# Kernel tuning notes

Hardware: AMD Instinct MI355X
Metric: run time of the kernel (lower is better)

The kernel has to match this reference:

```python
import jax, jax.numpy as jnp
import numpy as np

B = 32768
SEQ_LEN = 24
H = 64            # HIDDEN_DIM
SLOTS = 8         # MEMORY_SLOTS
VOCAB = 64        # VOCAB_SIZE


def setup_inputs() -> dict:
    key = jax.random.key(0)
    ks = jax.random.split(key, 8)
    seqs = jax.random.randint(ks[0], (B, SEQ_LEN), 0, VOCAB, dtype=jnp.int64)
    query_tok = jax.random.randint(ks[1], (B,), 0, VOCAB + 2, dtype=jnp.int64)
    embed = jax.random.normal(ks[2], (VOCAB + 2, H), dtype=jnp.float32) * 0.05
    gw1 = jax.random.normal(ks[3], (2 * H, 32), dtype=jnp.float32) / np.sqrt(2 * H)
    gb1 = jnp.zeros((32,), jnp.float32)
    gw2 = jax.random.normal(ks[4], (32, 1), dtype=jnp.float32) / np.sqrt(32)
    gb2 = jnp.zeros((1,), jnp.float32)
    rw1 = jax.random.normal(ks[5], (2 * H, H), dtype=jnp.float32) / np.sqrt(2 * H)
    rb1 = jnp.zeros((H,), jnp.float32)
    rw2 = jax.random.normal(ks[6], (H, VOCAB), dtype=jnp.float32) / np.sqrt(H)
    rb2 = jnp.zeros((VOCAB,), jnp.float32)
    return {"seqs": seqs, "query_tok": query_tok, "embed": embed,
            "gw1": gw1, "gb1": gb1, "gw2": gw2, "gb2": gb2,
            "rw1": rw1, "rb1": rb1, "rw2": rw2, "rb2": rb2}


def reference(seqs, query_tok, embed, gw1, gb1, gw2, gb2, rw1, rb1, rw2, rb2):
    Bb = seqs.shape[0]
    T = SEQ_LEN - 1  # model writes tokens 0..SEQ_LEN-2 into memory
    embs = embed[seqs[:, :T]]                     # [B, T, H]
    batch_idx = jnp.arange(Bb)

    def step(mem, xs):
        t, emb = xs                               # emb: [B, H]
        ctx = jnp.broadcast_to(emb[:, None, :], mem.shape)
        pair = jnp.concatenate([ctx, mem], axis=-1)        # [B, S, 2H]
        h = jax.nn.relu(pair @ gw1 + gb1)                  # [B, S, 32]
        score = jax.nn.sigmoid(h @ gw2 + gb2)[..., 0]      # [B, S]
        # while memory not full, fill slot t; otherwise evict argmax score
        idx = jnp.where(t < SLOTS, t, jnp.argmax(score, axis=1))
        mem = mem.at[batch_idx, idx].set(emb)
        return mem, None

    mem0 = jnp.zeros((Bb, SLOTS, H), embed.dtype)
    mem, _ = jax.lax.scan(step, mem0, (jnp.arange(T), jnp.swapaxes(embs, 0, 1)))

    summary = mem.mean(axis=1)                    # [B, H]  (memory is full: T > SLOTS)
    q = embed[query_tok]                          # [B, H]
    x = jnp.concatenate([q, summary], axis=-1)    # [B, 2H]
    logits = jax.nn.relu(x @ rw1 + rb1) @ rw2 + rb2   # [B, VOCAB]
    return logits
```

## Files before the change

### kernel.cpp

```cpp
#include <hip/hip_runtime.h>
#include <math.h>

typedef __attribute__((ext_vector_type(8))) _Float16 f16x8;
typedef __attribute__((ext_vector_type(4))) float f32x4;

#define TSTEPS 23
#define ROWS 128

#define WSB_Z  0
#define WSB_B1 16384
#define WSB_W2 37888

__global__ __launch_bounds__(256) void pre_all(
    const float* __restrict__ embed, const float* __restrict__ gw1,
    const float* __restrict__ gb1, const float* __restrict__ gw2,
    const float* __restrict__ gb2, const float* __restrict__ rw1,
    const float* __restrict__ rb1, const float* __restrict__ rw2,
    char* __restrict__ wsc)
{
    __shared__ float sEmb[66 * 64];
    __shared__ float sW[128 * 64];
    __shared__ float sV[64 * 33];
    __shared__ float sU[4 * 32];
    __shared__ float sG[65];
    __shared__ float sRb1[64];

    const int tid = threadIdx.x;
    const int blk = blockIdx.x;

    if (blk < 16) {
        {
            const float4* es = (const float4*)embed;
            float4* ed = (float4*)sEmb;
            for (int i = tid; i < 1024; i += 256) ed[i] = es[i];
            const float4* gs = (const float4*)gw1;
            float4* gd = (float4*)sW;
            for (int i = tid; i < 1024; i += 256) gd[i] = gs[i];
            if (tid < 32) { sG[tid] = gb1[tid]; sG[32 + tid] = gw2[tid]; }
            if (tid == 64) sG[64] = gb2[0];
        }
        __syncthreads();
        {
            const int s = tid >> 2, j0 = (tid & 3) * 8;
            float4 er[16];
            const float4* erp = (const float4*)(sEmb + s * 64);
            #pragma unroll
            for (int q = 0; q < 16; ++q) er[q] = erp[q];
            float acc[8] = {0.f, 0.f, 0.f, 0.f, 0.f, 0.f, 0.f, 0.f};
            #pragma unroll
            for (int k = 0; k < 64; ++k) {
                const float ek = ((const float*)er)[k];
                const float4 w0 = *(const float4*)&sW[(64 + k) * 32 + j0];
                const float4 w1 = *(const float4*)&sW[(64 + k) * 32 + j0 + 4];
                acc[0] = fmaf(ek, w0.x, acc[0]); acc[1] = fmaf(ek, w0.y, acc[1]);
                acc[2] = fmaf(ek, w0.z, acc[2]); acc[3] = fmaf(ek, w0.w, acc[3]);
                acc[4] = fmaf(ek, w1.x, acc[4]); acc[5] = fmaf(ek, w1.y, acc[5]);
                acc[6] = fmaf(ek, w1.z, acc[6]); acc[7] = fmaf(ek, w1.w, acc[7]);
            }
            #pragma unroll
            for (int jj = 0; jj < 8; ++jj) sV[s * 33 + j0 + jj] = acc[jj];
        }
        if (tid < 128) {
            const int cc = tid >> 5, j = tid & 31;
            const int c = blk * 4 + cc;
            float acc = 0.f;
            const float* er = sEmb + c * 64;
            #pragma unroll
            for (int k = 0; k < 64; ++k)
                acc = fmaf(er[k], sW[k * 32 + j], acc);
            sU[cc * 32 + j] = acc;
        }
        __syncthreads();
        {
            const int cc = tid >> 6, s = tid & 63;
            const int c = blk * 4 + cc;
            double z = (double)sG[64];
            #pragma unroll
            for (int j = 0; j < 32; ++j) {
                const double a = (double)sU[cc * 32 + j] + (double)sV[s * 33 + j] + (double)sG[j];
                if (a > 0.0) z += a * (double)sG[32 + j];
            }
            ((float*)(wsc + WSB_Z))[c * 64 + s] = (float)(1.0 / (1.0 + exp(-z)));
        }
    } else if (blk < 49) {
        {
            const float4* es = (const float4*)embed;
            float4* ed = (float4*)sEmb;
            for (int i = tid; i < 1056; i += 256) ed[i] = es[i];
            const float4* rs = (const float4*)rw1;
            float4* rd = (float4*)sW;
            for (int i = tid; i < 2048; i += 256) rd[i] = rs[i];
            if (tid < 64) sRb1[tid] = rb1[tid];
        }
        __syncthreads();
        const int e = (blk - 16) * 256 + tid;
        if (e < 8320) {
            const int n = e & 63, k = e >> 6;
            const int trow = (k < 64) ? k : (k - 64);
            const int ofs = (k < 64) ? 64 : 0;
            float4 er[16];
            const float4* erp = (const float4*)(sEmb + trow * 64);
            #pragma unroll
            for (int q = 0; q < 16; ++q) er[q] = erp[q];
            float acc = (k < 64) ? 0.f : sRb1[n];
            #pragma unroll
            for (int m = 0; m < 64; ++m)
                acc = fmaf(((const float*)er)[m], sW[(ofs + m) * 64 + n], acc);
            acc *= (k < 64) ? (0.125f * 256.f) : 256.f;
            ((_Float16*)(wsc + WSB_B1))[n * 168 + k] = (_Float16)acc;
        }
    } else {
        _Float16* w2t = (_Float16*)(wsc + WSB_W2);
        for (int e = tid; e < 4096; e += 256) {
            const int n = e & 63, j = e >> 6;
            w2t[n * 72 + j] = (_Float16)rw2[j * 64 + n];
        }
        _Float16* b1 = (_Float16*)(wsc + WSB_B1);
        for (int e = tid; e < 2432; e += 256) {
            const int n = e / 38, k = 130 + (e - n * 38);
            b1[n * 168 + k] = (_Float16)0.f;
        }
    }
}

__device__ __forceinline__ f16x8 build_slot_win(const unsigned* s, const unsigned* hb, int ko)
{
    unsigned w0 = 0, w1 = 0, w2 = 0, w3 = 0;
    #pragma unroll
    for (int i = 0; i < 8; ++i) {
        const unsigned d = s[i] - (unsigned)ko;
        const unsigned val = (d < 8u) ? (hb[i] << ((d & 1u) * 16)) : 0u;
        const unsigned q = d >> 1;
        w0 |= (q == 0u) ? val : 0u;
        w1 |= (q == 1u) ? val : 0u;
        w2 |= (q == 2u) ? val : 0u;
        w3 |= (q == 3u) ? val : 0u;
    }
    union { unsigned u[4]; f16x8 v; } r;
    r.u[0] = w0; r.u[1] = w1; r.u[2] = w2; r.u[3] = w3;
    return r.v;
}

__device__ __forceinline__ f16x8 build_q_win(int kq, int ko)
{
    const unsigned d = (unsigned)(kq - ko);
    const unsigned val = (d < 8u) ? (0x3C00u << ((d & 1u) * 16)) : 0u;
    const unsigned q = d >> 1;
    union { unsigned u[4]; f16x8 v; } r;
    r.u[0] = (q == 0u) ? val : 0u;
    r.u[1] = (q == 1u) ? val : 0u;
    r.u[2] = (q == 2u) ? val : 0u;
    r.u[3] = (q == 3u) ? val : 0u;
    return r.v;
}

#define L_Z    0
#define L_B1   16384
#define L_W2   37888
#define L_H    47104
#define L_ROW  65536
#define L_RB2  67584

__global__ __launch_bounds__(512, 4) void sm_main(
    const int* __restrict__ seqs, const int* __restrict__ qtok,
    const float* __restrict__ rb2, const char* __restrict__ wsc,
    float* __restrict__ out)
{
    __shared__ __align__(16) char smem[67840];
    float*    sZ   = (float*)(smem + L_Z);
    _Float16* sB1  = (_Float16*)(smem + L_B1);
    _Float16* sW2  = (_Float16*)(smem + L_W2);
    _Float16* sH   = (_Float16*)(smem + L_H);
    uint4*    sRow = (uint4*)(smem + L_ROW);
    float*    sRb2 = (float*)(smem + L_RB2);

    const int tid = threadIdx.x;
    const int base = blockIdx.x * ROWS;

    unsigned pk[6];
    int qt = 0;
    if (tid < ROWS) {
        const int4* sq = (const int4*)(seqs + (size_t)(base + tid) * 24);
        #pragma unroll
        for (int i = 0; i < 6; ++i) {
            const int4 w4 = sq[i];
            pk[i] = (unsigned)w4.x | ((unsigned)w4.y << 8) |
                    ((unsigned)w4.z << 16) | ((unsigned)w4.w << 24);
        }
        qt = qtok[base + tid];
    }

    {
        const float4* zsrc = (const float4*)(wsc + WSB_Z);
        float4* zdst = (float4*)sZ;
        for (int i = tid; i < 1024; i += 512) zdst[i] = zsrc[i];
        const float4* b1s = (const float4*)(wsc + WSB_B1);
        float4* b1d = (float4*)sB1;
        for (int i = tid; i < 1344; i += 512) b1d[i] = b1s[i];
        const float4* w2s = (const float4*)(wsc + WSB_W2);
        float4* w2d = (float4*)sW2;
        for (int i = tid; i < 576; i += 512) w2d[i] = w2s[i];
        if (tid < 64) sRb2[tid] = rb2[tid];
    }
    __syncthreads();

    if (tid < ROWS) {
        unsigned lo = pk[0], hi = pk[1];
        #pragma unroll
        for (int t = 8; t < TSTEPS; ++t) {
            const int c = (int)((pk[t >> 2] >> ((t & 3) * 8)) & 255u);
            const float* zr = sZ + c * 64;
            float b = zr[lo & 63]; int am = 0; float z;
            z = zr[(lo >> 8) & 63];  if (z > b) { b = z; am = 1; }
            z = zr[(lo >> 16) & 63]; if (z > b) { b = z; am = 2; }
            z = zr[lo >> 24];        if (z > b) { b = z; am = 3; }
            z = zr[hi & 63];         if (z > b) { b = z; am = 4; }
            z = zr[(hi >> 8) & 63];  if (z > b) { b = z; am = 5; }
            z = zr[(hi >> 16) & 63]; if (z > b) { b = z; am = 6; }
            z = zr[hi >> 24];        if (z > b) { b = z; am = 7; }
            const unsigned cb = (unsigned)c;
            if (am < 4) { const int sh = am * 8; lo = (lo & ~(255u << sh)) | (cb << sh); }
            else        { const int sh = am * 8 - 32; hi = (hi & ~(255u << sh)) | (cb << sh); }
        }
        int t_[8] = { (int)(lo & 63), (int)((lo >> 8) & 63), (int)((lo >> 16) & 63), (int)(lo >> 24),
                      (int)(hi & 63), (int)((hi >> 8) & 63), (int)((hi >> 16) & 63), (int)(hi >> 24) };
        int tot[8] = {1, 1, 1, 1, 1, 1, 1, 1};
        #pragma unroll
        for (int i = 0; i < 8; ++i)
            #pragma unroll
            for (int j = i + 1; j < 8; ++j) {
                const int eq = (t_[i] == t_[j]);
                tot[i] += eq; tot[j] += eq;
            }
        unsigned tp = 0;
        #pragma unroll
        for (int i = 0; i < 8; ++i) tp |= (unsigned)tot[i] << (4 * i);
        sRow[tid] = make_uint4(lo & 0x3F3F3F3Fu, hi & 0x3F3F3F3Fu, tp, (unsigned)qt);
    }
    __syncthreads();

    const int lane = tid & 63;
    const int w = tid >> 6;
    const int c16 = lane & 15, g = lane >> 4;
    const int arow = w * 16 + c16;

    unsigned sl[8], hb[8];
    int kq;
    {
        const uint4 ri = sRow[arow];
        sl[0] = ri.x & 63u; sl[1] = (ri.x >> 8) & 63u;
        sl[2] = (ri.x >> 16) & 63u; sl[3] = ri.x >> 24;
        sl[4] = ri.y & 63u; sl[5] = (ri.y >> 8) & 63u;
        sl[6] = (ri.y >> 16) & 63u; sl[7] = ri.y >> 24;
        #pragma unroll
        for (int i = 0; i < 8; ++i) {
            const unsigned tot = (ri.z >> (4 * i)) & 15u;
            union { _Float16 h; unsigned short b; } cv;
            cv.h = (_Float16)(float)tot;
            hb[i] = (unsigned)cv.b;
        }
        kq = 64 + (int)ri.w;
    }

    f32x4 a0 = {0.f, 0.f, 0.f, 0.f}, a1 = a0, a2 = a0, a3 = a0;
    #pragma unroll
    for (int ks = 0; ks < 5; ++ks) {
        const int ko = ks * 32 + g * 8;
        const f16x8 af = (ks < 2) ? build_slot_win(sl, hb, ko) : build_q_win(kq, ko);
        const f16x8 b0 = *(const f16x8*)&sB1[(c16) * 168 + ko];
        const f16x8 b1 = *(const f16x8*)&sB1[(16 + c16) * 168 + ko];
        const f16x8 b2 = *(const f16x8*)&sB1[(32 + c16) * 168 + ko];
        const f16x8 b3 = *(const f16x8*)&sB1[(48 + c16) * 168 + ko];
        a0 = __builtin_amdgcn_mfma_f32_16x16x32_f16(af, b0, a0, 0, 0, 0);
        a1 = __builtin_amdgcn_mfma_f32_16x16x32_f16(af, b1, a1, 0, 0, 0);
        a2 = __builtin_amdgcn_mfma_f32_16x16x32_f16(af, b2, a2, 0, 0, 0);
        a3 = __builtin_amdgcn_mfma_f32_16x16x32_f16(af, b3, a3, 0, 0, 0);
    }
    {
        const int rbase = w * 16 + g * 4;
        #pragma unroll
        for (int j = 0; j < 4; ++j) {
            _Float16* hr = sH + (rbase + j) * 72;
            const float v0 = a0[j], v1 = a1[j], v2 = a2[j], v3 = a3[j];
            hr[c16]      = (_Float16)(v0 > 0.f ? v0 : 0.f);
            hr[16 + c16] = (_Float16)(v1 > 0.f ? v1 : 0.f);
            hr[32 + c16] = (_Float16)(v2 > 0.f ? v2 : 0.f);
            hr[48 + c16] = (_Float16)(v3 > 0.f ? v3 : 0.f);
        }
    }
    __syncthreads();

    f32x4 d0 = {0.f, 0.f, 0.f, 0.f}, d1 = d0, d2 = d0, d3 = d0;
    #pragma unroll
    for (int ks = 0; ks < 2; ++ks) {
        const int ko = ks * 32 + g * 8;
        const f16x8 af = *(const f16x8*)&sH[arow * 72 + ko];
        const f16x8 b0 = *(const f16x8*)&sW2[(c16) * 72 + ko];
        const f16x8 b1 = *(const f16x8*)&sW2[(16 + c16) * 72 + ko];
        const f16x8 b2 = *(const f16x8*)&sW2[(32 + c16) * 72 + ko];
        const f16x8 b3 = *(const f16x8*)&sW2[(48 + c16) * 72 + ko];
        d0 = __builtin_amdgcn_mfma_f32_16x16x32_f16(af, b0, d0, 0, 0, 0);
        d1 = __builtin_amdgcn_mfma_f32_16x16x32_f16(af, b1, d1, 0, 0, 0);
        d2 = __builtin_amdgcn_mfma_f32_16x16x32_f16(af, b2, d2, 0, 0, 0);
        d3 = __builtin_amdgcn_mfma_f32_16x16x32_f16(af, b3, d3, 0, 0, 0);
    }
    float* sOut = (float*)(void*)smem;
    {
        const int rbase = w * 16 + g * 4;
        #pragma unroll
        for (int j = 0; j < 4; ++j) {
            float* orow = sOut + (rbase + j) * 68;
            orow[c16]      = d0[j] * (1.f / 256.f) + sRb2[c16];
            orow[16 + c16] = d1[j] * (1.f / 256.f) + sRb2[16 + c16];
            orow[32 + c16] = d2[j] * (1.f / 256.f) + sRb2[32 + c16];
            orow[48 + c16] = d3[j] * (1.f / 256.f) + sRb2[48 + c16];
        }
    }
    __syncthreads();

    #pragma unroll
    for (int r2 = 0; r2 < 4; ++r2) {
        const int idx = r2 * 512 + tid;
        const int row = idx >> 4, c4 = idx & 15;
        *(float4*)(out + (size_t)(base + row) * 64 + c4 * 4) =
            *(const float4*)&sOut[row * 68 + c4 * 4];
    }
}

extern "C" void kernel_launch(void* const* d_in, const int* in_sizes, int n_in,
                              void* d_out, int out_size, void* d_ws, size_t ws_size,
                              hipStream_t stream)
{
    const int* seqs    = (const int*)d_in[0];
    const int* qtok    = (const int*)d_in[1];
    const float* embed = (const float*)d_in[2];
    const float* gw1   = (const float*)d_in[3];
    const float* gb1   = (const float*)d_in[4];
    const float* gw2   = (const float*)d_in[5];
    const float* gb2   = (const float*)d_in[6];
    const float* rw1   = (const float*)d_in[7];
    const float* rb1   = (const float*)d_in[8];
    const float* rw2   = (const float*)d_in[9];
    const float* rb2   = (const float*)d_in[10];
    char* wsc  = (char*)d_ws;
    float* out = (float*)d_out;
    const int B = in_sizes[1];

    pre_all<<<50, 256, 0, stream>>>(embed, gw1, gb1, gw2, gb2, rw1, rb1, rw2, wsc);
    sm_main<<<B / ROWS, 512, 0, stream>>>(seqs, qtok, rb2, wsc, out);
}
```

Baseline: 21.44 us.

## Split gate-score precompute into two kernels and overlap weight staging with eviction scan

The gate-score table precompute is split in two. The first kernel computes the per-token U and V projections with one thread per output. A second small kernel combines them into the score table with four independent double accumulators, and it stores the pre-sigmoid logit, which keeps the same argmax ordering. In the main kernel only the score table is loaded before the first barrier, and the idle threads 128-511 stage the MLP weights while the first 128 threads run the eviction scan. This adds one more kernel launch in exchange for a shorter dependency chain and less serialized loading.

After: 22.30 us. 1.04x slower.

```diff
diff --git a/kernel.cpp b/kernel.cpp
--- a/kernel.cpp
+++ b/kernel.cpp
@@ -7,22 +7,19 @@
 #define TSTEPS 23
 #define ROWS 128
 
-#define WSB_Z  0
-#define WSB_B1 16384
-#define WSB_W2 37888
-
-__global__ __launch_bounds__(256) void pre_all(
+#define WSB_B1 0
+#define WSB_W2 21504
+#define WSB_U  30720
+#define WSB_V  38912
+#define WSB_Z  47104
+
+__global__ __launch_bounds__(256) void pre_lite(
     const float* __restrict__ embed, const float* __restrict__ gw1,
-    const float* __restrict__ gb1, const float* __restrict__ gw2,
-    const float* __restrict__ gb2, const float* __restrict__ rw1,
-    const float* __restrict__ rb1, const float* __restrict__ rw2,
-    char* __restrict__ wsc)
+    const float* __restrict__ rw1, const float* __restrict__ rb1,
+    const float* __restrict__ rw2, char* __restrict__ wsc)
 {
     __shared__ float sEmb[66 * 64];
     __shared__ float sW[128 * 64];
-    __shared__ float sV[64 * 33];
-    __shared__ float sU[4 * 32];
-    __shared__ float sG[65];
     __shared__ float sRb1[64];
 
     const int tid = threadIdx.x;
@@ -32,56 +29,22 @@
         {
             const float4* es = (const float4*)embed;
             float4* ed = (float4*)sEmb;
-            for (int i = tid; i < 1024; i += 256) ed[i] = es[i];
+            for (int i = tid; i < 1056; i += 256) ed[i] = es[i];
             const float4* gs = (const float4*)gw1;
             float4* gd = (float4*)sW;
             for (int i = tid; i < 1024; i += 256) gd[i] = gs[i];
-            if (tid < 32) { sG[tid] = gb1[tid]; sG[32 + tid] = gw2[tid]; }
-            if (tid == 64) sG[64] = gb2[0];
         }
         __syncthreads();
-        {
-            const int s = tid >> 2, j0 = (tid & 3) * 8;
-            float4 er[16];
-            const float4* erp = (const float4*)(sEmb + s * 64);
-            #pragma unroll
-            for (int q = 0; q < 16; ++q) er[q] = erp[q];
-            float acc[8] = {0.f, 0.f, 0.f, 0.f, 0.f, 0.f, 0.f, 0.f};
-            #pragma unroll
-            for (int k = 0; k < 64; ++k) {
-                const float ek = ((const float*)er)[k];
-                const float4 w0 = *(const float4*)&sW[(64 + k) * 32 + j0];
-                const float4 w1 = *(const float4*)&sW[(64 + k) * 32 + j0 + 4];
-                acc[0] = fmaf(ek, w0.x, acc[0]); acc[1] = fmaf(ek, w0.y, acc[1]);
-                acc[2] = fmaf(ek, w0.z, acc[2]); acc[3] = fmaf(ek, w0.w, acc[3]);
-                acc[4] = fmaf(ek, w1.x, acc[4]); acc[5] = fmaf(ek, w1.y, acc[5]);
-                acc[6] = fmaf(ek, w1.z, acc[6]); acc[7] = fmaf(ek, w1.w, acc[7]);
-            }
-            #pragma unroll
-            for (int jj = 0; jj < 8; ++jj) sV[s * 33 + j0 + jj] = acc[jj];
-        }
-        if (tid < 128) {
-            const int cc = tid >> 5, j = tid & 31;
-            const int c = blk * 4 + cc;
-            float acc = 0.f;
-            const float* er = sEmb + c * 64;
-            #pragma unroll
-            for (int k = 0; k < 64; ++k)
-                acc = fmaf(er[k], sW[k * 32 + j], acc);
-            sU[cc * 32 + j] = acc;
-        }
-        __syncthreads();
-        {
-            const int cc = tid >> 6, s = tid & 63;
-            const int c = blk * 4 + cc;
-            double z = (double)sG[64];
-            #pragma unroll
-            for (int j = 0; j < 32; ++j) {
-                const double a = (double)sU[cc * 32 + j] + (double)sV[s * 33 + j] + (double)sG[j];
-                if (a > 0.0) z += a * (double)sG[32 + j];
-            }
-            ((float*)(wsc + WSB_Z))[c * 64 + s] = (float)(1.0 / (1.0 + exp(-z)));
-        }
+        const int e = blk * 256 + tid;
+        const int row = (e >> 5) & 63, j = e & 31;
+        const int ofs = (e < 2048) ? 0 : 64;
+        float acc = 0.f;
+        const float* er = sEmb + row * 64;
+        #pragma unroll
+        for (int k = 0; k < 64; ++k)
+            acc = fmaf(er[k], sW[(ofs + k) * 32 + j], acc);
+        float* dst = (float*)(wsc + ((e < 2048) ? WSB_U : WSB_V));
+        dst[e & 2047] = acc;
     } else if (blk < 49) {
         {
             const float4* es = (const float4*)embed;
@@ -123,6 +86,48 @@
     }
 }
 
+__global__ __launch_bounds__(256) void pre_z2(
+    const float* __restrict__ gb1, const float* __restrict__ gw2,
+    const float* __restrict__ gb2, char* __restrict__ wsc)
+{
+    __shared__ float sU[64 * 33];
+    __shared__ float sV[64 * 33];
+    __shared__ float sG1[32];
+    __shared__ float sG2[32];
+
+    const int tid = threadIdx.x;
+    const float* u = (const float*)(wsc + WSB_U);
+    const float* v = (const float*)(wsc + WSB_V);
+    for (int i = tid; i < 2048; i += 256) {
+        sU[(i >> 5) * 33 + (i & 31)] = u[i];
+        sV[(i >> 5) * 33 + (i & 31)] = v[i];
+    }
+    if (tid < 32) { sG1[tid] = gb1[tid]; sG2[tid] = gw2[tid]; }
+    __syncthreads();
+
+    const int idx = blockIdx.x * 256 + tid;
+    const int c = idx >> 6, s = idx & 63;
+
+    float ur[32], vr[32];
+    #pragma unroll
+    for (int j = 0; j < 32; ++j) { ur[j] = sU[c * 33 + j]; vr[j] = sV[s * 33 + j]; }
+
+    double p0 = 0.0, p1 = 0.0, p2 = 0.0, p3 = 0.0;
+    #pragma unroll
+    for (int j = 0; j < 32; j += 4) {
+        const double a0 = (double)ur[j]     + (double)vr[j]     + (double)sG1[j];
+        const double a1 = (double)ur[j + 1] + (double)vr[j + 1] + (double)sG1[j + 1];
+        const double a2 = (double)ur[j + 2] + (double)vr[j + 2] + (double)sG1[j + 2];
+        const double a3 = (double)ur[j + 3] + (double)vr[j + 3] + (double)sG1[j + 3];
+        if (a0 > 0.0) p0 += a0 * (double)sG2[j];
+        if (a1 > 0.0) p1 += a1 * (double)sG2[j + 1];
+        if (a2 > 0.0) p2 += a2 * (double)sG2[j + 2];
+        if (a3 > 0.0) p3 += a3 * (double)sG2[j + 3];
+    }
+    const double z = (double)gb2[0] + ((p0 + p1) + (p2 + p3));
+    ((float*)(wsc + WSB_Z))[idx] = (float)z;
+}
+
 __device__ __forceinline__ f16x8 build_slot_win(const unsigned* s, const unsigned* hb, int ko)
 {
     unsigned w0 = 0, w1 = 0, w2 = 0, w3 = 0;
@@ -193,13 +198,8 @@
     {
         const float4* zsrc = (const float4*)(wsc + WSB_Z);
         float4* zdst = (float4*)sZ;
-        for (int i = tid; i < 1024; i += 512) zdst[i] = zsrc[i];
-        const float4* b1s = (const float4*)(wsc + WSB_B1);
-        float4* b1d = (float4*)sB1;
-        for (int i = tid; i < 1344; i += 512) b1d[i] = b1s[i];
-        const float4* w2s = (const float4*)(wsc + WSB_W2);
-        float4* w2d = (float4*)sW2;
-        for (int i = tid; i < 576; i += 512) w2d[i] = w2s[i];
+        #pragma unroll
+        for (int i = 0; i < 2; ++i) zdst[tid + i * 512] = zsrc[tid + i * 512];
         if (tid < 64) sRb2[tid] = rb2[tid];
     }
     __syncthreads();
@@ -236,6 +236,14 @@
         #pragma unroll
         for (int i = 0; i < 8; ++i) tp |= (unsigned)tot[i] << (4 * i);
         sRow[tid] = make_uint4(lo & 0x3F3F3F3Fu, hi & 0x3F3F3F3Fu, tp, (unsigned)qt);
+    } else {
+        const int t2 = tid - 128;
+        const float4* b1s = (const float4*)(wsc + WSB_B1);
+        float4* b1d = (float4*)sB1;
+        for (int i = t2; i < 1344; i += 384) b1d[i] = b1s[i];
+        const float4* w2s = (const float4*)(wsc + WSB_W2);
+        float4* w2d = (float4*)sW2;
+        for (int i = t2; i < 576; i += 384) w2d[i] = w2s[i];
     }
     __syncthreads();
 
@@ -346,6 +354,7 @@
     float* out = (float*)d_out;
     const int B = in_sizes[1];
 
-    pre_all<<<50, 256, 0, stream>>>(embed, gw1, gb1, gw2, gb2, rw1, rb1, rw2, wsc);
+    pre_lite<<<50, 256, 0, stream>>>(embed, gw1, rw1, rb1, rw2, wsc);
+    pre_z2<<<16, 256, 0, stream>>>(gb1, gw2, gb2, wsc);
     sm_main<<<B / ROWS, 512, 0, stream>>>(seqs, qtok, rb2, wsc, out);
 }
```

## Overlap weight staging with eviction scan and store pre-sigmoid scores

Applied to the files above, without the earlier changes.

The main kernel now loads only the score table before the first barrier. The B1 and W2 weight tiles are copied into shared memory by the 384 threads that sit idle during the per-row eviction scan, which hides that load latency behind the scan. The precompute kernel writes the raw logit instead of the sigmoid, which keeps the argmax order since sigmoid is monotonic. It also splits the double-precision reduction into four accumulators and reorders the workspace offsets. The split reduction changes summation order, which could flip near-tied argmax results.

After: 19.54 us. 1.1x faster.

```diff
diff --git a/kernel.cpp b/kernel.cpp
--- a/kernel.cpp
+++ b/kernel.cpp
@@ -7,9 +7,9 @@
 #define TSTEPS 23
 #define ROWS 128
 
-#define WSB_Z  0
-#define WSB_B1 16384
-#define WSB_W2 37888
+#define WSB_B1 0
+#define WSB_W2 21504
+#define WSB_Z  30720
 
 __global__ __launch_bounds__(256) void pre_all(
     const float* __restrict__ embed, const float* __restrict__ gw1,
@@ -58,7 +58,7 @@
                 acc[6] = fmaf(ek, w1.z, acc[6]); acc[7] = fmaf(ek, w1.w, acc[7]);
             }
             #pragma unroll
-            for (int jj = 0; jj < 8; ++jj) sV[s * 33 + j0 + jj] = acc[jj];
+            for (int jj = 0; jj < 8; ++jj) sV[s * 33 + jj + j0] = acc[jj];
         }
         if (tid < 128) {
             const int cc = tid >> 5, j = tid & 31;
@@ -74,13 +74,23 @@
         {
             const int cc = tid >> 6, s = tid & 63;
             const int c = blk * 4 + cc;
-            double z = (double)sG[64];
-            #pragma unroll
-            for (int j = 0; j < 32; ++j) {
-                const double a = (double)sU[cc * 32 + j] + (double)sV[s * 33 + j] + (double)sG[j];
-                if (a > 0.0) z += a * (double)sG[32 + j];
+            float ur[32], vr[32];
+            #pragma unroll
+            for (int j = 0; j < 32; ++j) { ur[j] = sU[cc * 32 + j]; vr[j] = sV[s * 33 + j]; }
+            double p0 = 0.0, p1 = 0.0, p2 = 0.0, p3 = 0.0;
+            #pragma unroll
+            for (int j = 0; j < 32; j += 4) {
+                const double a0 = (double)ur[j]     + (double)vr[j]     + (double)sG[j];
+                const double a1 = (double)ur[j + 1] + (double)vr[j + 1] + (double)sG[j + 1];
+                const double a2 = (double)ur[j + 2] + (double)vr[j + 2] + (double)sG[j + 2];
+                const double a3 = (double)ur[j + 3] + (double)vr[j + 3] + (double)sG[j + 3];
+                if (a0 > 0.0) p0 += a0 * (double)sG[32 + j];
+                if (a1 > 0.0) p1 += a1 * (double)sG[32 + j + 1];
+                if (a2 > 0.0) p2 += a2 * (double)sG[32 + j + 2];
+                if (a3 > 0.0) p3 += a3 * (double)sG[32 + j + 3];
             }
-            ((float*)(wsc + WSB_Z))[c * 64 + s] = (float)(1.0 / (1.0 + exp(-z)));
+            const double z = (double)sG[64] + ((p0 + p1) + (p2 + p3));
+            ((float*)(wsc + WSB_Z))[c * 64 + s] = (float)z;
         }
     } else if (blk < 49) {
         {
@@ -193,13 +203,8 @@
     {
         const float4* zsrc = (const float4*)(wsc + WSB_Z);
         float4* zdst = (float4*)sZ;
-        for (int i = tid; i < 1024; i += 512) zdst[i] = zsrc[i];
-        const float4* b1s = (const float4*)(wsc + WSB_B1);
-        float4* b1d = (float4*)sB1;
-        for (int i = tid; i < 1344; i += 512) b1d[i] = b1s[i];
-        const float4* w2s = (const float4*)(wsc + WSB_W2);
-        float4* w2d = (float4*)sW2;
-        for (int i = tid; i < 576; i += 512) w2d[i] = w2s[i];
+        #pragma unroll
+        for (int i = 0; i < 2; ++i) zdst[tid + i * 512] = zsrc[tid + i * 512];
         if (tid < 64) sRb2[tid] = rb2[tid];
     }
     __syncthreads();
@@ -236,6 +241,14 @@
         #pragma unroll
         for (int i = 0; i < 8; ++i) tp |= (unsigned)tot[i] << (4 * i);
         sRow[tid] = make_uint4(lo & 0x3F3F3F3Fu, hi & 0x3F3F3F3Fu, tp, (unsigned)qt);
+    } else {
+        const int t2 = tid - 128;
+        const float4* b1s = (const float4*)(wsc + WSB_B1);
+        float4* b1d = (float4*)sB1;
+        for (int i = t2; i < 1344; i += 384) b1d[i] = b1s[i];
+        const float4* w2s = (const float4*)(wsc + WSB_W2);
+        float4* w2d = (float4*)sW2;
+        for (int i = t2; i < 576; i += 384) w2d[i] = w2s[i];
     }
     __syncthreads();
 
```
